# Optimization experiments

Measured on AMD Instinct MI355X. Metric: run time of the kernel, lower is better.

## Reference

```python
import jax, jax.numpy as jnp
import numpy as np

N_NODES = 75000
N_EDGES = 1200000
DIM = 64


def setup_inputs() -> dict:
    key = jax.random.key(0)
    ks = jax.random.split(key, 9)
    d_u = jax.random.normal(ks[0], (N_NODES, DIM), dtype=jnp.float32)
    p_u = jax.random.normal(ks[1], (N_NODES, DIM), dtype=jnp.float32)
    s = 1.0 / np.sqrt(DIM)
    w_q = jax.random.normal(ks[2], (DIM, DIM), dtype=jnp.float32) * s
    w_k = jax.random.normal(ks[3], (DIM, DIM), dtype=jnp.float32) * s
    w_v = jax.random.normal(ks[4], (DIM, DIM), dtype=jnp.float32) * s
    e1 = jax.random.normal(ks[5], (DIM,), dtype=jnp.float32) * s
    e2 = jax.random.normal(ks[6], (DIM,), dtype=jnp.float32) * s
    src = jax.random.randint(ks[7], (N_EDGES,), 0, N_NODES, dtype=jnp.int32)
    dst = jax.random.randint(ks[8], (N_EDGES,), 0, N_NODES, dtype=jnp.int32)
    return {"d_u": d_u, "p_u": p_u, "w_q": w_q, "w_k": w_k, "w_v": w_v,
            "e1": e1, "e2": e2, "src": src, "dst": dst}


def reference(d_u, p_u, w_q, w_k, w_v, e1, e2, src, dst):
    n_nodes = d_u.shape[0]
    # per-node edge scores: e1(w_k(p_u)) on src side, e2(w_q(d_u)) on dst side
    h_src = (p_u @ w_k.T) @ e1            # [N]
    h_dst = (d_u @ w_q.T) @ e2            # [N]
    # apply_edges(u_add_v): c_e = h_src[u] + h_dst[v], shape [E]
    c = h_src[src] + h_dst[dst]
    # EdgeWeightNorm(norm='right'): divide by sum of incoming edge weights at dst
    denom = jax.ops.segment_sum(c, dst, num_segments=n_nodes)  # [N]
    c = c / denom[dst]
    # update_all(u_mul_e, sum): messages w_v(p_u)[u] * c_e, summed at dst
    wv = p_u @ w_v.T                      # [N, D]
    msg = wv[src] * c[:, None]            # [E, D]
    out = jax.ops.segment_sum(msg, dst, num_segments=n_nodes)  # [N, D]
    return out
```

## Files before the change

### kernel.cpp

```cpp
#include <hip/hip_runtime.h>

#define N_NODES 75000
#define N_EDGES 1200000
#define DIM 64
#define SCAN_BLK 1024
#define N_SCAN_BLKS ((N_NODES + SCAN_BLK - 1) / SCAN_BLK)
#define NCOPY 8
#define HIST_BLKS 1172
#define NW_BLKS 586
#define FAT_BLKS (HIST_BLKS + NW_BLKS)

__device__ __forceinline__ float lane_bcf(float v, int l) {
    return __int_as_float(__builtin_amdgcn_readlane(__float_as_int(v), l));
}
__device__ __forceinline__ int lane_bci(int v, int l) {
    return __builtin_amdgcn_readlane(v, l);
}

__global__ __launch_bounds__(256, 4) void fat_kernel(
    const int* __restrict__ dst, int* __restrict__ cnt8, int* __restrict__ rank,
    const float* __restrict__ d_u, const float* __restrict__ p_u,
    const float* __restrict__ w_v, const float* __restrict__ w_q,
    const float* __restrict__ w_k,
    const float* __restrict__ e1, const float* __restrict__ e2,
    double* __restrict__ h_src, double* __restrict__ h_dst,
    float* __restrict__ wv_out) {

    int b = blockIdx.x;
    int g = b / 3;
    int r = b - 3 * g;

    if (r < 2) {
        int hb = 2 * g + r;
        int xcc;
        asm volatile("s_getreg_b32 %0, hwreg(HW_REG_XCC_ID)" : "=s"(xcc));
        xcc &= (NCOPY - 1);
        int* mycnt = cnt8 + (size_t)xcc * N_NODES;
        int tag = xcc << 28;
        int base = hb << 10;
        #pragma unroll
        for (int k = 0; k < 4; ++k) {
            int e = base + k * 256 + threadIdx.x;
            if (e < N_EDGES) {
                int rr = atomicAdd(&mycnt[dst[e]], 1);
                rank[e] = rr | tag;
            }
        }
        return;
    }

    __shared__ double al_sh[DIM];
    __shared__ double bl_sh[DIM];
    int lane = threadIdx.x & 63;

    if (threadIdx.x < DIM) {
        double al = 0.0, bl = 0.0;
        #pragma unroll 8
        for (int j = 0; j < DIM; ++j) {
            al += (double)e1[j] * (double)w_k[j * DIM + threadIdx.x];
            bl += (double)e2[j] * (double)w_q[j * DIM + threadIdx.x];
        }
        al_sh[threadIdx.x] = al;
        bl_sh[threadIdx.x] = bl;
    }

    float w[DIM];
    const float4* wr = (const float4*)(w_v + (size_t)lane * DIM);
    #pragma unroll
    for (int k = 0; k < DIM / 4; ++k) {
        float4 v = wr[k];
        w[4 * k + 0] = v.x; w[4 * k + 1] = v.y;
        w[4 * k + 2] = v.z; w[4 * k + 3] = v.w;
    }
    __syncthreads();
    double al = al_sh[lane];
    double bl = bl_sh[lane];

    int wave = (g * 256 + threadIdx.x) >> 6;
    int nwaves = NW_BLKS * 4;

    for (int i = wave; i < N_NODES; i += nwaves) {
        float pl = p_u[(size_t)i * DIM + lane];
        float dl = d_u[(size_t)i * DIM + lane];

        double hs = (double)pl * al;
        #pragma unroll
        for (int off = 32; off > 0; off >>= 1) hs += __shfl_xor(hs, off, 64);
        double hd = (double)dl * bl;
        #pragma unroll
        for (int off = 32; off > 0; off >>= 1) hd += __shfl_xor(hd, off, 64);
        if (lane == 0) { h_src[i] = hs; h_dst[i] = hd; }

        float a0 = 0.f, a1 = 0.f, a2 = 0.f, a3 = 0.f;
        #pragma unroll
        for (int d = 0; d < DIM; d += 4) {
            a0 += w[d + 0] * lane_bcf(pl, d + 0);
            a1 += w[d + 1] * lane_bcf(pl, d + 1);
            a2 += w[d + 2] * lane_bcf(pl, d + 2);
            a3 += w[d + 3] * lane_bcf(pl, d + 3);
        }
        wv_out[(size_t)i * DIM + lane] = (a0 + a1) + (a2 + a3);
    }
}

__global__ __launch_bounds__(SCAN_BLK) void scan_kernel(
    int* __restrict__ cnt8, int* __restrict__ cnt,
    int* __restrict__ row, unsigned int* __restrict__ pub) {
    __shared__ int sh[SCAN_BLK];
    __shared__ int bpref;
    int tid = threadIdx.x;
    int i = blockIdx.x * SCAN_BLK + tid;
    int v = 0;
    if (i < N_NODES) {
        int run = 0;
        #pragma unroll
        for (int c = 0; c < NCOPY; ++c) {
            int x = cnt8[(size_t)c * N_NODES + i];
            cnt8[(size_t)c * N_NODES + i] = run;
            run += x;
        }
        v = run;
        cnt[i] = run;
    }
    sh[tid] = v;
    __syncthreads();
    for (int off = 1; off < SCAN_BLK; off <<= 1) {
        int t = (tid >= off) ? sh[tid - off] : 0;
        __syncthreads();
        sh[tid] += t;
        __syncthreads();
    }
    int incl = sh[tid];
    if (tid == SCAN_BLK - 1)
        atomicExch(&pub[blockIdx.x], (unsigned)incl | 0x80000000u);
    if (tid < 64) {
        int s = 0;
        for (int l = tid; l < (int)blockIdx.x; l += 64) {
            unsigned x;
            do { x = atomicAdd(&pub[l], 0u); } while (!(x & 0x80000000u));
            s += (int)(x & 0x7FFFFFFFu);
        }
        #pragma unroll
        for (int off = 32; off > 0; off >>= 1) s += __shfl_xor(s, off, 64);
        if (tid == 0) bpref = s;
    }
    __syncthreads();
    if (i < N_NODES) row[i] = bpref + incl - v;
}

__global__ __launch_bounds__(256) void build_kernel(
    const int* __restrict__ src, const int* __restrict__ dst,
    const int* __restrict__ row, const int* __restrict__ cnt8,
    const int* __restrict__ rank, int* __restrict__ csr_src) {
    int e = blockIdx.x * 256 + threadIdx.x;
    if (e >= N_EDGES) return;
    int d = dst[e];
    int rp = rank[e];
    int copy = (rp >> 28) & (NCOPY - 1);
    int r = rp & 0x0FFFFFFF;
    int pos = row[d] + cnt8[(size_t)copy * N_NODES + d] + r;
    __builtin_nontemporal_store(src[e], &csr_src[pos]);
}

__global__ __launch_bounds__(256) void node_gather(
    const int* __restrict__ row, const int* __restrict__ cnt,
    const int* __restrict__ csr_src,
    const double* __restrict__ h_src, const double* __restrict__ h_dst,
    const float* __restrict__ wv, float* __restrict__ out) {
    int gtid = blockIdx.x * 256 + threadIdx.x;
    int node = gtid >> 6;
    int lane = threadIdx.x & 63;
    if (node >= N_NODES) return;

    int start = row[node];
    int deg = cnt[node];
    double hd = h_dst[node];

    if (deg <= 64) {
        int s0 = 0;
        double c0 = 0.0;
        if (lane < deg) {
            s0 = csr_src[start + lane];
            c0 = h_src[s0] + hd;
        }
        double r = c0;
        if (deg > 32) r += __shfl_xor(r, 32, 64);
        if (deg > 16) r += __shfl_xor(r, 16, 64);
        r += __shfl_xor(r, 8, 64);
        r += __shfl_xor(r, 4, 64);
        r += __shfl_xor(r, 2, 64);
        r += __shfl_xor(r, 1, 64);
        double inv = 1.0 / r;
        float cf0 = (lane < deg) ? (float)(c0 * inv) : 0.f;

        int g = lane >> 4;
        int sub = lane & 15;
        float ax = 0.f, ay = 0.f, az = 0.f, aw = 0.f;
        int rounds = (deg + 3) >> 2;
        int j = 0;
        for (; j + 2 <= rounds; j += 2) {
            int l0 = 4 * j + g;
            int l1 = l0 + 4;
            int   sA = __shfl(s0, l0, 64);
            float cA = __shfl(cf0, l0, 64);
            int   sB = __shfl(s0, l1, 64);
            float cB = __shfl(cf0, l1, 64);
            float4 vA = ((const float4*)(wv + (size_t)sA * DIM))[sub];
            float4 vB = ((const float4*)(wv + (size_t)sB * DIM))[sub];
            ax += vA.x * cA; ay += vA.y * cA; az += vA.z * cA; aw += vA.w * cA;
            ax += vB.x * cB; ay += vB.y * cB; az += vB.z * cB; aw += vB.w * cB;
        }
        if (j < rounds) {
            int l0 = 4 * j + g;
            int   sA = __shfl(s0, l0, 64);
            float cA = __shfl(cf0, l0, 64);
            float4 vA = ((const float4*)(wv + (size_t)sA * DIM))[sub];
            ax += vA.x * cA; ay += vA.y * cA; az += vA.z * cA; aw += vA.w * cA;
        }
        ax += __shfl_xor(ax, 16, 64); ay += __shfl_xor(ay, 16, 64);
        az += __shfl_xor(az, 16, 64); aw += __shfl_xor(aw, 16, 64);
        ax += __shfl_xor(ax, 32, 64); ay += __shfl_xor(ay, 32, 64);
        az += __shfl_xor(az, 32, 64); aw += __shfl_xor(aw, 32, 64);
        if (g == 0) {
            float4 o; o.x = ax; o.y = ay; o.z = az; o.w = aw;
            ((float4*)(out + (size_t)node * DIM))[sub] = o;
        }
    } else {
        double denom = 0.0;
        for (int base = 0; base < deg; base += 64) {
            int m = deg - base; if (m > 64) m = 64;
            double c = 0.0;
            if (lane < m) {
                int s = csr_src[start + base + lane];
                c = h_src[s] + hd;
            }
            #pragma unroll
            for (int off = 32; off > 0; off >>= 1) c += __shfl_xor(c, off, 64);
            denom += c;
        }
        double inv = 1.0 / denom;
        float acc = 0.f;
        for (int base = 0; base < deg; base += 64) {
            int m = deg - base; if (m > 64) m = 64;
            int s1 = 0; float cf1 = 0.f;
            if (lane < m) {
                s1 = csr_src[start + base + lane];
                cf1 = (float)((h_src[s1] + hd) * inv);
            }
            for (int j = 0; j < m; ++j) {
                int s = lane_bci(s1, j);
                float cf = lane_bcf(cf1, j);
                acc += wv[(size_t)s * DIM + lane] * cf;
            }
        }
        out[(size_t)node * DIM + lane] = acc;
    }
}

extern "C" void kernel_launch(void* const* d_in, const int* in_sizes, int n_in,
                              void* d_out, int out_size, void* d_ws, size_t ws_size,
                              hipStream_t stream) {
    const float* d_u = (const float*)d_in[0];
    const float* p_u = (const float*)d_in[1];
    const float* w_q = (const float*)d_in[2];
    const float* w_k = (const float*)d_in[3];
    const float* w_v = (const float*)d_in[4];
    const float* e1  = (const float*)d_in[5];
    const float* e2  = (const float*)d_in[6];
    const int*   src = (const int*)d_in[7];
    const int*   dst = (const int*)d_in[8];
    float* out = (float*)d_out;

    double* h_src  = (double*)d_ws;
    double* h_dst  = h_src + N_NODES;
    float*  wv     = (float*)(h_dst + N_NODES);
    int*    cnt    = (int*)(wv + (size_t)N_NODES * DIM);
    int*    row    = cnt + N_NODES;
    int*    cnt8   = row + N_NODES;
    unsigned int* pub = (unsigned int*)(cnt8 + (size_t)NCOPY * N_NODES);
    int*    rank   = (int*)pub + 128;
    int*    csr_src= rank + N_EDGES;

    hipMemsetAsync(cnt8, 0, sizeof(int) * ((size_t)NCOPY * N_NODES + 128),
                   stream);

    fat_kernel<<<FAT_BLKS, 256, 0, stream>>>(
        dst, cnt8, rank, d_u, p_u, w_v, w_q, w_k, e1, e2, h_src, h_dst, wv);

    scan_kernel<<<N_SCAN_BLKS, SCAN_BLK, 0, stream>>>(cnt8, cnt, row, pub);

    build_kernel<<<(N_EDGES + 255) / 256, 256, 0, stream>>>(
        src, dst, row, cnt8, rank, csr_src);

    node_gather<<<(N_NODES * 64 + 255) / 256, 256, 0, stream>>>(
        row, cnt, csr_src, h_src, h_dst, wv, out);
}
```

Before: 272.2 us.

## Store projected node features in fp16 and split fused histogram/projection kernel

The w_v projection output is now stored as fp16, halving the bytes moved by the random per-edge gathers in node_gather, which reads 8 halves per lane in 8-lane groups. The fused kernel that interleaved histogram blocks with projection blocks is split into a separate hist_kernel and a node_wave kernel on a fixed 1024-block grid. This trades accuracy, since per-edge message values lose mantissa bits, for less gather bandwidth, and gives up the concurrent overlap of the two workloads in exchange for an extra launch.

```diff
diff --git a/kernel.cpp b/kernel.cpp
--- a/kernel.cpp
+++ b/kernel.cpp
@@ -6,9 +6,9 @@
 #define SCAN_BLK 1024
 #define N_SCAN_BLKS ((N_NODES + SCAN_BLK - 1) / SCAN_BLK)
 #define NCOPY 8
-#define HIST_BLKS 1172
-#define NW_BLKS 586
-#define FAT_BLKS (HIST_BLKS + NW_BLKS)
+#define HIST_BLKS ((N_EDGES + 1023) / 1024)
+
+typedef _Float16 half8 __attribute__((ext_vector_type(8)));
 
 __device__ __forceinline__ float lane_bcf(float v, int l) {
     return __int_as_float(__builtin_amdgcn_readlane(__float_as_int(v), l));
@@ -17,38 +17,32 @@
     return __builtin_amdgcn_readlane(v, l);
 }
 
-__global__ __launch_bounds__(256, 4) void fat_kernel(
-    const int* __restrict__ dst, int* __restrict__ cnt8, int* __restrict__ rank,
+__global__ __launch_bounds__(256) void hist_kernel(
+    const int* __restrict__ dst, int* __restrict__ cnt8,
+    int* __restrict__ rank) {
+    int xcc;
+    asm volatile("s_getreg_b32 %0, hwreg(HW_REG_XCC_ID)" : "=s"(xcc));
+    xcc &= (NCOPY - 1);
+    int* mycnt = cnt8 + (size_t)xcc * N_NODES;
+    int tag = xcc << 28;
+    int base = blockIdx.x << 10;
+    #pragma unroll
+    for (int k = 0; k < 4; ++k) {
+        int e = base + k * 256 + threadIdx.x;
+        if (e < N_EDGES) {
+            int r = atomicAdd(&mycnt[dst[e]], 1);
+            rank[e] = r | tag;
+        }
+    }
+}
+
+__global__ __launch_bounds__(256, 4) void node_wave(
     const float* __restrict__ d_u, const float* __restrict__ p_u,
     const float* __restrict__ w_v, const float* __restrict__ w_q,
     const float* __restrict__ w_k,
     const float* __restrict__ e1, const float* __restrict__ e2,
     double* __restrict__ h_src, double* __restrict__ h_dst,
-    float* __restrict__ wv_out) {
-
-    int b = blockIdx.x;
-    int g = b / 3;
-    int r = b - 3 * g;
-
-    if (r < 2) {
-        int hb = 2 * g + r;
-        int xcc;
-        asm volatile("s_getreg_b32 %0, hwreg(HW_REG_XCC_ID)" : "=s"(xcc));
-        xcc &= (NCOPY - 1);
-        int* mycnt = cnt8 + (size_t)xcc * N_NODES;
-        int tag = xcc << 28;
-        int base = hb << 10;
-        #pragma unroll
-        for (int k = 0; k < 4; ++k) {
-            int e = base + k * 256 + threadIdx.x;
-            if (e < N_EDGES) {
-                int rr = atomicAdd(&mycnt[dst[e]], 1);
-                rank[e] = rr | tag;
-            }
-        }
-        return;
-    }
-
+    _Float16* __restrict__ wvh) {
     __shared__ double al_sh[DIM];
     __shared__ double bl_sh[DIM];
     int lane = threadIdx.x & 63;
@@ -76,8 +70,8 @@
     double al = al_sh[lane];
     double bl = bl_sh[lane];
 
-    int wave = (g * 256 + threadIdx.x) >> 6;
-    int nwaves = NW_BLKS * 4;
+    int wave = (blockIdx.x * 256 + threadIdx.x) >> 6;
+    int nwaves = gridDim.x * 4;
 
     for (int i = wave; i < N_NODES; i += nwaves) {
         float pl = p_u[(size_t)i * DIM + lane];
@@ -99,7 +93,7 @@
             a2 += w[d + 2] * lane_bcf(pl, d + 2);
             a3 += w[d + 3] * lane_bcf(pl, d + 3);
         }
-        wv_out[(size_t)i * DIM + lane] = (a0 + a1) + (a2 + a3);
+        wvh[(size_t)i * DIM + lane] = (_Float16)((a0 + a1) + (a2 + a3));
     }
 }
 
@@ -166,7 +160,7 @@
     const int* __restrict__ row, const int* __restrict__ cnt,
     const int* __restrict__ csr_src,
     const double* __restrict__ h_src, const double* __restrict__ h_dst,
-    const float* __restrict__ wv, float* __restrict__ out) {
+    const _Float16* __restrict__ wvh, float* __restrict__ out) {
     int gtid = blockIdx.x * 256 + threadIdx.x;
     int node = gtid >> 6;
     int lane = threadIdx.x & 63;
@@ -193,37 +187,46 @@
         double inv = 1.0 / r;
         float cf0 = (lane < deg) ? (float)(c0 * inv) : 0.f;
 
-        int g = lane >> 4;
-        int sub = lane & 15;
-        float ax = 0.f, ay = 0.f, az = 0.f, aw = 0.f;
-        int rounds = (deg + 3) >> 2;
+        int g8 = lane >> 3;
+        int sub8 = lane & 7;
+        float ac[8];
+        #pragma unroll
+        for (int k = 0; k < 8; ++k) ac[k] = 0.f;
+
+        int rounds = (deg + 7) >> 3;
         int j = 0;
         for (; j + 2 <= rounds; j += 2) {
-            int l0 = 4 * j + g;
-            int l1 = l0 + 4;
+            int l0 = 8 * j + g8;
+            int l1 = l0 + 8;
             int   sA = __shfl(s0, l0, 64);
             float cA = __shfl(cf0, l0, 64);
             int   sB = __shfl(s0, l1, 64);
             float cB = __shfl(cf0, l1, 64);
-            float4 vA = ((const float4*)(wv + (size_t)sA * DIM))[sub];
-            float4 vB = ((const float4*)(wv + (size_t)sB * DIM))[sub];
-            ax += vA.x * cA; ay += vA.y * cA; az += vA.z * cA; aw += vA.w * cA;
-            ax += vB.x * cB; ay += vB.y * cB; az += vB.z * cB; aw += vB.w * cB;
+            half8 vA = ((const half8*)(wvh + (size_t)sA * DIM))[sub8];
+            half8 vB = ((const half8*)(wvh + (size_t)sB * DIM))[sub8];
+            #pragma unroll
+            for (int k = 0; k < 8; ++k) ac[k] += (float)vA[k] * cA;
+            #pragma unroll
+            for (int k = 0; k < 8; ++k) ac[k] += (float)vB[k] * cB;
         }
         if (j < rounds) {
-            int l0 = 4 * j + g;
+            int l0 = 8 * j + g8;
             int   sA = __shfl(s0, l0, 64);
             float cA = __shfl(cf0, l0, 64);
-            float4 vA = ((const float4*)(wv + (size_t)sA * DIM))[sub];
-            ax += vA.x * cA; ay += vA.y * cA; az += vA.z * cA; aw += vA.w * cA;
-        }
-        ax += __shfl_xor(ax, 16, 64); ay += __shfl_xor(ay, 16, 64);
-        az += __shfl_xor(az, 16, 64); aw += __shfl_xor(aw, 16, 64);
-        ax += __shfl_xor(ax, 32, 64); ay += __shfl_xor(ay, 32, 64);
-        az += __shfl_xor(az, 32, 64); aw += __shfl_xor(aw, 32, 64);
-        if (g == 0) {
-            float4 o; o.x = ax; o.y = ay; o.z = az; o.w = aw;
-            ((float4*)(out + (size_t)node * DIM))[sub] = o;
+            half8 vA = ((const half8*)(wvh + (size_t)sA * DIM))[sub8];
+            #pragma unroll
+            for (int k = 0; k < 8; ++k) ac[k] += (float)vA[k] * cA;
+        }
+        #pragma unroll
+        for (int off = 8; off < 64; off <<= 1) {
+            #pragma unroll
+            for (int k = 0; k < 8; ++k) ac[k] += __shfl_xor(ac[k], off, 64);
+        }
+        if (g8 == 0) {
+            float4* orow = (float4*)(out + (size_t)node * DIM + sub8 * 8);
+            float4 o0; o0.x = ac[0]; o0.y = ac[1]; o0.z = ac[2]; o0.w = ac[3];
+            float4 o1; o1.x = ac[4]; o1.y = ac[5]; o1.z = ac[6]; o1.w = ac[7];
+            orow[0] = o0; orow[1] = o1;
         }
     } else {
         double denom = 0.0;
@@ -250,7 +253,7 @@
             for (int j = 0; j < m; ++j) {
                 int s = lane_bci(s1, j);
                 float cf = lane_bcf(cf1, j);
-                acc += wv[(size_t)s * DIM + lane] * cf;
+                acc += (float)wvh[(size_t)s * DIM + lane] * cf;
             }
         }
         out[(size_t)node * DIM + lane] = acc;
@@ -273,8 +276,8 @@
 
     double* h_src  = (double*)d_ws;
     double* h_dst  = h_src + N_NODES;
-    float*  wv     = (float*)(h_dst + N_NODES);
-    int*    cnt    = (int*)(wv + (size_t)N_NODES * DIM);
+    _Float16* wvh  = (_Float16*)(h_dst + N_NODES);
+    int*    cnt    = (int*)(wvh + (size_t)N_NODES * DIM);
     int*    row    = cnt + N_NODES;
     int*    cnt8   = row + N_NODES;
     unsigned int* pub = (unsigned int*)(cnt8 + (size_t)NCOPY * N_NODES);
@@ -284,8 +287,10 @@
     hipMemsetAsync(cnt8, 0, sizeof(int) * ((size_t)NCOPY * N_NODES + 128),
                    stream);
 
-    fat_kernel<<<FAT_BLKS, 256, 0, stream>>>(
-        dst, cnt8, rank, d_u, p_u, w_v, w_q, w_k, e1, e2, h_src, h_dst, wv);
+    hist_kernel<<<HIST_BLKS, 256, 0, stream>>>(dst, cnt8, rank);
+
+    node_wave<<<1024, 256, 0, stream>>>(
+        d_u, p_u, w_v, w_q, w_k, e1, e2, h_src, h_dst, wvh);
 
     scan_kernel<<<N_SCAN_BLKS, SCAN_BLK, 0, stream>>>(cnt8, cnt, row, pub);
 
@@ -293,5 +298,5 @@
         src, dst, row, cnt8, rank, csr_src);
 
     node_gather<<<(N_NODES * 64 + 255) / 256, 256, 0, stream>>>(
-        row, cnt, csr_src, h_src, h_dst, wv, out);
-}
+        row, cnt, csr_src, h_src, h_dst, wvh, out);
+}
```

Measured after the change: 261.8 us. -3.8%, faster.
